# Performance work log

Hardware: AMD Instinct MI355X
Metric: run time of the kernel (lower is better)

Reference implementation:

```python
import jax, jax.numpy as jnp
import numpy as np


def setup_inputs() -> dict:
    key = jax.random.key(0)
    ks = jax.random.split(key, 8)
    B, Q, K, F, FV, C = 8, 2048, 2048, 512, 512, 2
    q = jax.random.normal(ks[0], (B, Q, F), dtype=jnp.float32)
    k = jax.random.normal(ks[1], (B, K, F), dtype=jnp.float32)
    v = jax.random.normal(ks[2], (B, K, FV), dtype=jnp.float32)
    coords_q = jax.random.uniform(ks[3], (B, Q, C), dtype=jnp.float32)
    coords_k = jax.random.uniform(ks[4], (B, K, C), dtype=jnp.float32)
    attn_mask = jax.random.randint(ks[5], (B, Q, K), 0, 2).astype(bool)
    alibi_mask = jax.random.randint(ks[6], (B, Q, K), 0, 2).astype(bool)
    bias_scale = jax.random.uniform(ks[7], (1,), dtype=jnp.float32)
    return {"q": q, "k": k, "v": v, "coords_q": coords_q, "coords_k": coords_k,
            "attn_mask": attn_mask, "alibi_mask": alibi_mask, "bias_scale": bias_scale}


def reference(q, k, v, coords_q, coords_k, attn_mask, alibi_mask, bias_scale):
    # scaled dot-product logits: [B, Q, K]
    scale = k.shape[-1] ** -0.5
    weight_logits = jnp.einsum('bqf,bkf->bqk', q, k) * scale
    # pairwise Euclidean coordinate distances: [B, Q, K]
    diff = coords_q[:, :, None, :] - coords_k[:, None, :, :]
    distances = jnp.linalg.norm(diff, axis=-1)
    # _RunningMeanScaler in eval mode divides by running_mean == 1 (identity)
    scaled_distances = distances * bias_scale  # bias_scale broadcasts from [1]
    scaled_distances = jnp.where(alibi_mask, 0.0, scaled_distances)
    weights = jax.nn.softmax(weight_logits, axis=-1)
    # post-softmax bias subtraction + masking (non-standard attention)
    weights = jnp.where(attn_mask, 0.0, weights - scaled_distances)
    attention = jnp.einsum('bqk,bkf->bqf', weights, v)
    return attention
```

## Files before the change

kernel.cpp:

```cpp
#include <hip/hip_runtime.h>
#include <hip/hip_bf16.h>
#include <math.h>

#define BN  8
#define QN  2048
#define KN  2048
#define FN  512
#define FVN 512

typedef __bf16 bf16x8 __attribute__((ext_vector_type(8)));
typedef __bf16 bf16x4v __attribute__((ext_vector_type(4)));
typedef float  f32x4  __attribute__((ext_vector_type(4)));

__device__ inline bf16x8 pack8(float4 a, float4 b) {
  bf16x8 r;
  r[0] = (__bf16)a.x; r[1] = (__bf16)a.y; r[2] = (__bf16)a.z; r[3] = (__bf16)a.w;
  r[4] = (__bf16)b.x; r[5] = (__bf16)b.y; r[6] = (__bf16)b.z; r[7] = (__bf16)b.w;
  return r;
}

__device__ __forceinline__ void g2l16(const __bf16* g, __bf16* l) {
  __builtin_amdgcn_global_load_lds(
      (const __attribute__((address_space(1))) void*)g,
      (__attribute__((address_space(3))) void*)l,
      16, 0, 0);
}

__global__ __launch_bounds__(256) void prep(
    const float* __restrict__ qm, const float* __restrict__ km,
    const float* __restrict__ vm,
    __bf16* __restrict__ qb, __bf16* __restrict__ kb, __bf16* __restrict__ Vt,
    float* __restrict__ sums) {
  const int tid = threadIdx.x;
  if (blockIdx.y == 0) {
    const size_t idx = ((size_t)blockIdx.x * 256 + tid) * 8;
    const float scale = 0.044194173824159216f;
    float4 a = *(const float4*)(qm + idx);
    float4 b = *(const float4*)(qm + idx + 4);
    a.x *= scale; a.y *= scale; a.z *= scale; a.w *= scale;
    b.x *= scale; b.y *= scale; b.z *= scale; b.w *= scale;
    *(bf16x8*)(qb + idx) = pack8(a, b);
  } else if (blockIdx.y == 1) {
    const size_t idx = ((size_t)blockIdx.x * 256 + tid) * 8;
    float4 a = *(const float4*)(km + idx);
    float4 b = *(const float4*)(km + idx + 4);
    *(bf16x8*)(kb + idx) = pack8(a, b);
  } else if (blockIdx.y == 2) {
    const int bx = blockIdx.x;
    if (bx >= (KN / 64) * (FVN / 64) * BN) return;
    const int b  = bx >> 8;
    const int f0 = ((bx >> 5) & 7) * 64;
    const int k0 = (bx & 31) * 64;
    __shared__ float tile[64][65];
    const int r = tid >> 4;
    const int c = (tid & 15) * 4;
#pragma unroll
    for (int i = 0; i < 4; i++) {
      float4 u = *(const float4*)(vm + ((size_t)b * KN + k0 + r + i * 16) * FVN + f0 + c);
      tile[r + i * 16][c] = u.x; tile[r + i * 16][c + 1] = u.y;
      tile[r + i * 16][c + 2] = u.z; tile[r + i * 16][c + 3] = u.w;
    }
    __syncthreads();
#pragma unroll
    for (int i = 0; i < 4; i++) {
      int fv = r + i * 16;
      bf16x4v w;
      w[0] = (__bf16)tile[c][fv];     w[1] = (__bf16)tile[c + 1][fv];
      w[2] = (__bf16)tile[c + 2][fv]; w[3] = (__bf16)tile[c + 3][fv];
      *(bf16x4v*)(Vt + ((size_t)b * FVN + f0 + fv) * KN + k0 + c) = w;
    }
  } else {
    if (blockIdx.x < (BN * QN) / 1024) {
      float4 z4; z4.x = 0.f; z4.y = 0.f; z4.z = 0.f; z4.w = 0.f;
      ((float4*)sums)[(size_t)blockIdx.x * 256 + tid] = z4;
    }
  }
}

__global__ __launch_bounds__(256) void gemm_s(
    const __bf16* __restrict__ qb, const __bf16* __restrict__ kb,
    __bf16* __restrict__ Sws, float* __restrict__ sums,
    int b0, int q0, int qchunk) {
  __shared__ __align__(16) __bf16 As[2][128][32];
  __shared__ __align__(16) __bf16 Bs[2][128][32];
  const int tid = threadIdx.x;
  const int lane = tid & 63, wave = tid >> 6;
  const int wq = (wave & 1) * 64, wk = (wave >> 1) * 64;
  const int qt = blockIdx.x * 128, kt = blockIdx.y * 128;
  const int z = blockIdx.z, b = b0 + z;
  __bf16* S = Sws + (size_t)z * qchunk * KN;
  const __bf16* Ab = qb + ((size_t)b * QN + q0 + qt) * FN;
  const __bf16* Bb = kb + ((size_t)b * KN + kt) * FN;
  const int srow = lane >> 2;
  const int scol = (lane & 3) * 8;
  const int r = lane & 15, quad = lane >> 4;
  f32x4 acc[4][4] = {};
  for (int f0 = 0; f0 < FN; f0 += 64) {
    __syncthreads();
#pragma unroll
    for (int h = 0; h < 2; h++) {
      const int co = f0 + h * 32 + scol;
      g2l16(Ab + (size_t)(wave * 32 + srow) * FN + co,      &As[h][wave * 32][0]);
      g2l16(Ab + (size_t)(wave * 32 + 16 + srow) * FN + co, &As[h][wave * 32 + 16][0]);
      g2l16(Bb + (size_t)(wave * 32 + srow) * FN + co,      &Bs[h][wave * 32][0]);
      g2l16(Bb + (size_t)(wave * 32 + 16 + srow) * FN + co, &Bs[h][wave * 32 + 16][0]);
    }
    __syncthreads();
#pragma unroll
    for (int h = 0; h < 2; h++) {
      bf16x8 af[4], bf[4];
#pragma unroll
      for (int i = 0; i < 4; i++) af[i] = *(bf16x8*)&As[h][wq + i * 16 + r][quad * 8];
#pragma unroll
      for (int j = 0; j < 4; j++) bf[j] = *(bf16x8*)&Bs[h][wk + j * 16 + r][quad * 8];
#pragma unroll
      for (int i = 0; i < 4; i++)
#pragma unroll
        for (int j = 0; j < 4; j++)
          acc[i][j] = __builtin_amdgcn_mfma_f32_16x16x32_bf16(af[i], bf[j], acc[i][j], 0, 0, 0);
    }
  }
#pragma unroll
  for (int i = 0; i < 4; i++)
#pragma unroll
    for (int j = 0; j < 4; j++)
#pragma unroll
      for (int t = 0; t < 4; t++) {
        int qq = qt + wq + i * 16 + quad * 4 + t;
        int kk = kt + wk + j * 16 + r;
        S[(size_t)qq * KN + kk] = (__bf16)acc[i][j][t];
      }
#pragma unroll
  for (int i = 0; i < 4; i++)
#pragma unroll
    for (int t = 0; t < 4; t++) {
      float part = 0.f;
#pragma unroll
      for (int j = 0; j < 4; j++) part += __expf(acc[i][j][t]);
      part += __shfl_xor(part, 1);
      part += __shfl_xor(part, 2);
      part += __shfl_xor(part, 4);
      part += __shfl_xor(part, 8);
      if (r == 0)
        atomicAdd(&sums[(size_t)b * QN + q0 + qt + wq + i * 16 + quad * 4 + t], part);
    }
}

__global__ __launch_bounds__(512) void gemm_wv(
    const __bf16* __restrict__ Sws, const __bf16* __restrict__ Vt,
    const float* __restrict__ sums,
    const float* __restrict__ cq, const float* __restrict__ ck,
    const int* __restrict__ attn, const int* __restrict__ alibi,
    const float* __restrict__ bsp, float* __restrict__ out,
    int b0, int q0, int qchunk, int nb) {
  __shared__ __align__(16) __bf16 As[2][64][32];
  __shared__ __align__(16) __bf16 Bs[2][512][32];
  const int tid = threadIdx.x;
  const int lane = tid & 63, wave = tid >> 6;
  const int flat = blockIdx.x;
  const int z = flat & (nb - 1);
  const int b = b0 + z;
  const int qt = (flat / nb) * 64;
  const int arow_i = tid >> 3;
  const int ac8 = tid & 7;
  const int qg = q0 + qt + arow_i;
  const __bf16* Srow = Sws + ((size_t)z * qchunk + qt + arow_i) * KN;
  const int* arow = attn + ((size_t)b * QN + qg) * KN;
  const int* lrow = alibi + ((size_t)b * QN + qg) * KN;
  const float* ckb = ck + (size_t)b * KN * 2;
  const float inv = 1.0f / sums[(size_t)b * QN + qg];
  const float qx = cq[((size_t)b * QN + qg) * 2 + 0];
  const float qy = cq[((size_t)b * QN + qg) * 2 + 1];
  const float bs = bsp[0];
  const int srow = tid >> 2;
  const int scol = (tid & 3) * 8;
  const __bf16* Bb = Vt + (size_t)b * FVN * KN;
  const int r = lane & 15, quad = lane >> 4;
  const int wq2 = (wave & 1) * 32;
  const int wf  = (wave >> 1) * 128;

  f32x4 acc[2][8] = {};
  bf16x8 s8; int4 am0, am1, al0, al1; float4 c0, c1, c2, c3;
  {
    const int kk = ac8 * 8;
    s8  = *(const bf16x8*)(Srow + kk);
    am0 = *(const int4*)(arow + kk); am1 = *(const int4*)(arow + kk + 4);
    al0 = *(const int4*)(lrow + kk); al1 = *(const int4*)(lrow + kk + 4);
    c0 = *(const float4*)(ckb + (size_t)kk * 2);
    c1 = *(const float4*)(ckb + (size_t)kk * 2 + 4);
    c2 = *(const float4*)(ckb + (size_t)kk * 2 + 8);
    c3 = *(const float4*)(ckb + (size_t)kk * 2 + 12);
  }
  for (int t = 0; t < KN / 64; ++t) {
    __syncthreads();
    {
      int   am[8] = {am0.x, am0.y, am0.z, am0.w, am1.x, am1.y, am1.z, am1.w};
      int   al[8] = {al0.x, al0.y, al0.z, al0.w, al1.x, al1.y, al1.z, al1.w};
      float kx[8] = {c0.x, c0.z, c1.x, c1.z, c2.x, c2.z, c3.x, c3.z};
      float ky[8] = {c0.y, c0.w, c1.y, c1.w, c2.y, c2.w, c3.y, c3.w};
      bf16x8 w8;
#pragma unroll
      for (int j = 0; j < 8; j++) {
        float p = __expf((float)s8[j]);
        float dx = qx - kx[j], dy = qy - ky[j];
        float sd = al[j] ? 0.f : sqrtf(dx * dx + dy * dy) * bs;
        float w = am[j] ? 0.f : (p * inv - sd);
        w8[j] = (__bf16)w;
      }
      *(bf16x8*)&As[ac8 >> 2][arow_i][(ac8 & 3) * 8] = w8;
    }
    const int k0 = t * 64;
#pragma unroll
    for (int h = 0; h < 2; h++)
#pragma unroll
      for (int rr = 0; rr < 4; rr++)
        g2l16(Bb + (size_t)(rr * 128 + srow) * KN + k0 + h * 32 + scol,
              &Bs[h][rr * 128 + wave * 16][0]);
    __syncthreads();
    if (t + 1 < KN / 64) {
      const int kk = (t + 1) * 64 + ac8 * 8;
      s8  = *(const bf16x8*)(Srow + kk);
      am0 = *(const int4*)(arow + kk); am1 = *(const int4*)(arow + kk + 4);
      al0 = *(const int4*)(lrow + kk); al1 = *(const int4*)(lrow + kk + 4);
      c0 = *(const float4*)(ckb + (size_t)kk * 2);
      c1 = *(const float4*)(ckb + (size_t)kk * 2 + 4);
      c2 = *(const float4*)(ckb + (size_t)kk * 2 + 8);
      c3 = *(const float4*)(ckb + (size_t)kk * 2 + 12);
    }
#pragma unroll
    for (int h = 0; h < 2; h++) {
      bf16x8 af[2], bv[8];
#pragma unroll
      for (int i = 0; i < 2; i++) af[i] = *(bf16x8*)&As[h][wq2 + i * 16 + r][quad * 8];
#pragma unroll
      for (int j = 0; j < 8; j++) bv[j] = *(bf16x8*)&Bs[h][wf + j * 16 + r][quad * 8];
#pragma unroll
      for (int i = 0; i < 2; i++)
#pragma unroll
        for (int j = 0; j < 8; j++)
          acc[i][j] = __builtin_amdgcn_mfma_f32_16x16x32_bf16(af[i], bv[j], acc[i][j], 0, 0, 0);
    }
  }
#pragma unroll
  for (int i = 0; i < 2; i++)
#pragma unroll
    for (int j = 0; j < 8; j++)
#pragma unroll
      for (int t4 = 0; t4 < 4; t4++) {
        int qq = q0 + qt + wq2 + i * 16 + quad * 4 + t4;
        int fv = wf + j * 16 + r;
        out[((size_t)b * QN + qq) * FVN + fv] = acc[i][j][t4];
      }
}

extern "C" void kernel_launch(void* const* d_in, const int* in_sizes, int n_in,
                              void* d_out, int out_size, void* d_ws, size_t ws_size,
                              hipStream_t stream) {
  (void)in_sizes; (void)n_in; (void)out_size;
  const float* qm   = (const float*)d_in[0];
  const float* km   = (const float*)d_in[1];
  const float* vm   = (const float*)d_in[2];
  const float* cq   = (const float*)d_in[3];
  const float* ck   = (const float*)d_in[4];
  const int*   attn = (const int*)d_in[5];
  const int*   alibi= (const int*)d_in[6];
  const float* bsp  = (const float*)d_in[7];
  float* out = (float*)d_out;

  __bf16* qb  = (__bf16*)d_ws;
  __bf16* kb  = qb + (size_t)BN * QN * FN;
  __bf16* Vt  = kb + (size_t)BN * KN * FN;
  float*  sums = (float*)(Vt + (size_t)BN * FVN * KN);
  __bf16* Sws = (__bf16*)(sums + (size_t)BN * QN);
  const size_t fixed = ((size_t)BN * QN * FN + (size_t)BN * KN * FN +
                        (size_t)BN * FVN * KN) * 2 + (size_t)BN * QN * 4;
  int nb = BN, qc = QN;
  while (nb > 1 && fixed + (size_t)nb * qc * KN * 2 > ws_size) nb >>= 1;
  while (qc > 128 && fixed + (size_t)nb * qc * KN * 2 > ws_size) qc >>= 1;

  prep<<<dim3((BN * QN * FN) / 2048, 4), 256, 0, stream>>>(qm, km, vm, qb, kb, Vt, sums);
  for (int b0 = 0; b0 < BN; b0 += nb) {
    for (int q0 = 0; q0 < QN; q0 += qc) {
      gemm_s<<<dim3(qc / 128, KN / 128, nb), 256, 0, stream>>>(qb, kb, Sws, sums, b0, q0, qc);
      gemm_wv<<<dim3(nb * (qc / 64)), 512, 0, stream>>>(Sws, Vt, sums, cq, ck, attn,
                                                        alibi, bsp, out, b0, q0, qc, nb);
    }
  }
}
```

Baseline: 499.6 us.

## Replace LDS-staged weight·V GEMM with direct-register MFMA operands and XCD swizzle

```diff
diff --git a/kernel.cpp b/kernel.cpp
--- a/kernel.cpp
+++ b/kernel.cpp
@@ -146,54 +146,49 @@
     }
 }
 
-__global__ __launch_bounds__(512) void gemm_wv(
+__global__ __launch_bounds__(256) void gemm_wd(
     const __bf16* __restrict__ Sws, const __bf16* __restrict__ Vt,
     const float* __restrict__ sums,
     const float* __restrict__ cq, const float* __restrict__ ck,
     const int* __restrict__ attn, const int* __restrict__ alibi,
     const float* __restrict__ bsp, float* __restrict__ out,
-    int b0, int q0, int qchunk, int nb) {
-  __shared__ __align__(16) __bf16 As[2][64][32];
-  __shared__ __align__(16) __bf16 Bs[2][512][32];
+    int b0, int q0, int qchunk) {
+  const int nqt = qchunk / 32;
+  const int nwg = gridDim.x;
+  int work = blockIdx.x;
+  if ((nwg & 7) == 0)
+    work = (work & 7) * (nwg >> 3) + (work >> 3);
+  const int z = work / nqt, qt = work % nqt;
+  const int b = b0 + z;
   const int tid = threadIdx.x;
-  const int lane = tid & 63, wave = tid >> 6;
-  const int flat = blockIdx.x;
-  const int z = flat & (nb - 1);
-  const int b = b0 + z;
-  const int qt = (flat / nb) * 64;
-  const int arow_i = tid >> 3;
-  const int ac8 = tid & 7;
-  const int qg = q0 + qt + arow_i;
-  const __bf16* Srow = Sws + ((size_t)z * qchunk + qt + arow_i) * KN;
+  const int lane = tid & 63;
+  const int wave = tid >> 6;
+  const int r = lane & 15, quad = lane >> 4;
+  const int wq = (wave >> 1) * 16;
+  const int wf = (wave & 1) * 256;
+  const int qrow_l = qt * 32 + wq + r;
+  const int qg = q0 + qrow_l;
+  const __bf16* Srow = Sws + ((size_t)z * qchunk + qrow_l) * KN;
   const int* arow = attn + ((size_t)b * QN + qg) * KN;
   const int* lrow = alibi + ((size_t)b * QN + qg) * KN;
   const float* ckb = ck + (size_t)b * KN * 2;
+  const __bf16* Vb = Vt + ((size_t)b * FVN + wf + r) * KN;
   const float inv = 1.0f / sums[(size_t)b * QN + qg];
   const float qx = cq[((size_t)b * QN + qg) * 2 + 0];
   const float qy = cq[((size_t)b * QN + qg) * 2 + 1];
   const float bs = bsp[0];
-  const int srow = tid >> 2;
-  const int scol = (tid & 3) * 8;
-  const __bf16* Bb = Vt + (size_t)b * FVN * KN;
-  const int r = lane & 15, quad = lane >> 4;
-  const int wq2 = (wave & 1) * 32;
-  const int wf  = (wave >> 1) * 128;
-
-  f32x4 acc[2][8] = {};
-  bf16x8 s8; int4 am0, am1, al0, al1; float4 c0, c1, c2, c3;
-  {
-    const int kk = ac8 * 8;
-    s8  = *(const bf16x8*)(Srow + kk);
-    am0 = *(const int4*)(arow + kk); am1 = *(const int4*)(arow + kk + 4);
-    al0 = *(const int4*)(lrow + kk); al1 = *(const int4*)(lrow + kk + 4);
-    c0 = *(const float4*)(ckb + (size_t)kk * 2);
-    c1 = *(const float4*)(ckb + (size_t)kk * 2 + 4);
-    c2 = *(const float4*)(ckb + (size_t)kk * 2 + 8);
-    c3 = *(const float4*)(ckb + (size_t)kk * 2 + 12);
-  }
-  for (int t = 0; t < KN / 64; ++t) {
-    __syncthreads();
-    {
+  f32x4 acc[16] = {};
+  for (int k0 = 0; k0 < KN; k0 += 64) {
+#pragma unroll
+    for (int h = 0; h < 2; h++) {
+      const int kk = k0 + h * 32 + quad * 8;
+      bf16x8 s8 = *(const bf16x8*)(Srow + kk);
+      int4 am0 = *(const int4*)(arow + kk), am1 = *(const int4*)(arow + kk + 4);
+      int4 al0 = *(const int4*)(lrow + kk), al1 = *(const int4*)(lrow + kk + 4);
+      float4 c0 = *(const float4*)(ckb + (size_t)kk * 2);
+      float4 c1 = *(const float4*)(ckb + (size_t)kk * 2 + 4);
+      float4 c2 = *(const float4*)(ckb + (size_t)kk * 2 + 8);
+      float4 c3 = *(const float4*)(ckb + (size_t)kk * 2 + 12);
       int   am[8] = {am0.x, am0.y, am0.z, am0.w, am1.x, am1.y, am1.z, am1.w};
       int   al[8] = {al0.x, al0.y, al0.z, al0.w, al1.x, al1.y, al1.z, al1.w};
       float kx[8] = {c0.x, c0.z, c1.x, c1.z, c2.x, c2.z, c3.x, c3.z};
@@ -201,56 +196,26 @@
       bf16x8 w8;
 #pragma unroll
       for (int j = 0; j < 8; j++) {
-        float p = __expf((float)s8[j]);
+        float p = __expf((float)s8[j]) * inv;
         float dx = qx - kx[j], dy = qy - ky[j];
         float sd = al[j] ? 0.f : sqrtf(dx * dx + dy * dy) * bs;
-        float w = am[j] ? 0.f : (p * inv - sd);
-        w8[j] = (__bf16)w;
+        w8[j] = (__bf16)(am[j] ? 0.f : (p - sd));
       }
-      *(bf16x8*)&As[ac8 >> 2][arow_i][(ac8 & 3) * 8] = w8;
-    }
-    const int k0 = t * 64;
-#pragma unroll
-    for (int h = 0; h < 2; h++)
-#pragma unroll
-      for (int rr = 0; rr < 4; rr++)
-        g2l16(Bb + (size_t)(rr * 128 + srow) * KN + k0 + h * 32 + scol,
-              &Bs[h][rr * 128 + wave * 16][0]);
-    __syncthreads();
-    if (t + 1 < KN / 64) {
-      const int kk = (t + 1) * 64 + ac8 * 8;
-      s8  = *(const bf16x8*)(Srow + kk);
-      am0 = *(const int4*)(arow + kk); am1 = *(const int4*)(arow + kk + 4);
-      al0 = *(const int4*)(lrow + kk); al1 = *(const int4*)(lrow + kk + 4);
-      c0 = *(const float4*)(ckb + (size_t)kk * 2);
-      c1 = *(const float4*)(ckb + (size_t)kk * 2 + 4);
-      c2 = *(const float4*)(ckb + (size_t)kk * 2 + 8);
-      c3 = *(const float4*)(ckb + (size_t)kk * 2 + 12);
-    }
-#pragma unroll
-    for (int h = 0; h < 2; h++) {
-      bf16x8 af[2], bv[8];
-#pragma unroll
-      for (int i = 0; i < 2; i++) af[i] = *(bf16x8*)&As[h][wq2 + i * 16 + r][quad * 8];
-#pragma unroll
-      for (int j = 0; j < 8; j++) bv[j] = *(bf16x8*)&Bs[h][wf + j * 16 + r][quad * 8];
-#pragma unroll
-      for (int i = 0; i < 2; i++)
-#pragma unroll
-        for (int j = 0; j < 8; j++)
-          acc[i][j] = __builtin_amdgcn_mfma_f32_16x16x32_bf16(af[i], bv[j], acc[i][j], 0, 0, 0);
-    }
-  }
-#pragma unroll
-  for (int i = 0; i < 2; i++)
-#pragma unroll
-    for (int j = 0; j < 8; j++)
-#pragma unroll
-      for (int t4 = 0; t4 < 4; t4++) {
-        int qq = q0 + qt + wq2 + i * 16 + quad * 4 + t4;
-        int fv = wf + j * 16 + r;
-        out[((size_t)b * QN + qq) * FVN + fv] = acc[i][j][t4];
+#pragma unroll
+      for (int j = 0; j < 16; j++) {
+        bf16x8 bv = *(const bf16x8*)(Vb + (size_t)j * 16 * KN + kk);
+        acc[j] = __builtin_amdgcn_mfma_f32_16x16x32_bf16(w8, bv, acc[j], 0, 0, 0);
       }
+    }
+  }
+#pragma unroll
+  for (int j = 0; j < 16; j++)
+#pragma unroll
+    for (int t = 0; t < 4; t++) {
+      int qq = q0 + qt * 32 + wq + quad * 4 + t;
+      int fv = wf + j * 16 + r;
+      out[((size_t)b * QN + qq) * FVN + fv] = acc[j][t];
+    }
 }
 
 extern "C" void kernel_launch(void* const* d_in, const int* in_sizes, int n_in,
@@ -282,8 +247,8 @@
   for (int b0 = 0; b0 < BN; b0 += nb) {
     for (int q0 = 0; q0 < QN; q0 += qc) {
       gemm_s<<<dim3(qc / 128, KN / 128, nb), 256, 0, stream>>>(qb, kb, Sws, sums, b0, q0, qc);
-      gemm_wv<<<dim3(nb * (qc / 64)), 512, 0, stream>>>(Sws, Vt, sums, cq, ck, attn,
-                                                        alibi, bsp, out, b0, q0, qc, nb);
-    }
-  }
-}
+      gemm_wd<<<dim3(nb * (qc / 32)), 256, 0, stream>>>(Sws, Vt, sums, cq, ck, attn,
+                                                        alibi, bsp, out, b0, q0, qc);
+    }
+  }
+}
```

After: 706.0 us. 41.3% more time.
